# Optimization experiments

Hardware: AMD Instinct MI355X
Metric: run time of the kernel (lower is better)

## Reference

```python
import jax, jax.numpy as jnp
import numpy as np

MODEL_DIM = 1024
N_HEADS = 16
HEAD_DIM = 64  # q_dim == k_dim == v_dim


def setup_inputs() -> dict:
    key = jax.random.key(0)
    ks = jax.random.split(key, 7)
    B, S = 4, 2048
    scale = 1.0 / np.sqrt(MODEL_DIM)
    return {
        "q": jax.random.normal(ks[0], (B, S, MODEL_DIM), dtype=jnp.float32),
        "k": jax.random.normal(ks[1], (B, S, MODEL_DIM), dtype=jnp.float32),
        "v": jax.random.normal(ks[2], (B, S, MODEL_DIM), dtype=jnp.float32),
        # Linear weights stored as [out, in] like torch; no biases.
        "wq": jax.random.normal(ks[3], (N_HEADS * HEAD_DIM, MODEL_DIM), dtype=jnp.float32) * scale,
        "wk": jax.random.normal(ks[4], (N_HEADS * HEAD_DIM, MODEL_DIM), dtype=jnp.float32) * scale,
        "wv": jax.random.normal(ks[5], (N_HEADS * HEAD_DIM, MODEL_DIM), dtype=jnp.float32) * scale,
        "wo": jax.random.normal(ks[6], (MODEL_DIM, N_HEADS * HEAD_DIM), dtype=jnp.float32) * scale,
    }


def reference(q, k, v, wq, wk, wv, wo):
    B, Sq, _ = q.shape
    Sk = k.shape[1]
    # projections: [B,S,D] @ W^T -> [B,S,H*dh] -> [B,H,S,dh]
    qh = (q @ wq.T).reshape(B, Sq, N_HEADS, HEAD_DIM).transpose(0, 2, 1, 3)
    kh = (k @ wk.T).reshape(B, Sk, N_HEADS, HEAD_DIM).transpose(0, 2, 1, 3)
    vh = (v @ wv.T).reshape(B, Sk, N_HEADS, HEAD_DIM).transpose(0, 2, 1, 3)
    # scores [B,H,Sq,Sk], scaled by sqrt(k_dim)
    scores = jnp.einsum('bhqd,bhkd->bhqk', qh, kh) / jnp.sqrt(jnp.float32(HEAD_DIM))
    attn = jax.nn.softmax(scores, axis=-1)
    ctx = jnp.einsum('bhqk,bhkd->bhqd', attn, vh)  # [B,H,Sq,dh]
    ctx = ctx.transpose(0, 2, 1, 3).reshape(B, Sq, N_HEADS * HEAD_DIM)
    return ctx @ wo.T
```

## Files before the change

kernel.cpp:

```cpp
#include <hip/hip_runtime.h>
#include <cstdint>
#include <cstddef>


typedef _Float16 f16x8 __attribute__((ext_vector_type(8)));
typedef _Float16 f16x4 __attribute__((ext_vector_type(4)));
typedef _Float16 f16x2 __attribute__((ext_vector_type(2)));
typedef __fp16 h16x2 __attribute__((ext_vector_type(2)));
typedef float f32x4 __attribute__((ext_vector_type(4)));
typedef float f32x16 __attribute__((ext_vector_type(16)));
typedef unsigned u32x4 __attribute__((ext_vector_type(4)));
typedef int i32x2 __attribute__((ext_vector_type(2)));

#define LDS_CAST(p) ((__attribute__((address_space(3))) void*)(p))
#define GLB_CAST(p) ((const __attribute__((address_space(1))) void*)(p))

__device__ __forceinline__ void gload_lds16(const void* g, void* l) {
  __builtin_amdgcn_global_load_lds(GLB_CAST(g), LDS_CAST(l), 16, 0, 0);
}

__device__ __forceinline__ float fexp2(float x) {
#if __has_builtin(__builtin_amdgcn_exp2f)
  return __builtin_amdgcn_exp2f(x);
#else
  return exp2f(x);
#endif
}

__device__ __forceinline__ f16x2 pkrtz(float a, float b) {
  h16x2 r = __builtin_amdgcn_cvt_pkrtz(a, b);
  return __builtin_bit_cast(f16x2, r);
}

__device__ __forceinline__ float dot2acc(f16x2 a, float acc) {
#if __has_builtin(__builtin_amdgcn_fdot2)
  const f16x2 one2 = {(_Float16)1.0f, (_Float16)1.0f};
  return __builtin_amdgcn_fdot2(a, one2, acc, false);
#else
  return acc + (float)a[0] + (float)a[1];
#endif
}

__device__ __forceinline__ void pl32swap(unsigned& a, unsigned& b) {
#if __has_builtin(__builtin_amdgcn_permlane32_swap)
  i32x2 r = __builtin_amdgcn_permlane32_swap((int)a, (int)b, false, false);
  a = (unsigned)r[0];
  b = (unsigned)r[1];
#else
  asm("v_permlane32_swap_b32 %0, %1" : "+v"(a), "+v"(b));
#endif
}

__global__ void cvt_all(const float* __restrict__ q, const float* __restrict__ k,
                        const float* __restrict__ v, const float* __restrict__ wq,
                        const float* __restrict__ wk, const float* __restrict__ wv,
                        const float* __restrict__ wo, _Float16* __restrict__ oq,
                        _Float16* __restrict__ ok, _Float16* __restrict__ ov,
                        _Float16* __restrict__ owq, _Float16* __restrict__ owk,
                        _Float16* __restrict__ owv, _Float16* __restrict__ owo) {
  int id = blockIdx.x;
  const float* in;
  _Float16* out;
  int base;
  if (id < 24576) {
    int z = id >> 13;
    base = (id & 8191) * 256;
    in = z == 0 ? q : z == 1 ? k : v;
    out = z == 0 ? oq : z == 1 ? ok : ov;
  } else {
    int id2 = id - 24576;
    int z = id2 >> 10;
    base = (id2 & 1023) * 256;
    in = z == 0 ? wq : z == 1 ? wk : z == 2 ? wv : wo;
    out = z == 0 ? owq : z == 1 ? owk : z == 2 ? owv : owo;
  }
  int i = base + threadIdx.x;
  float4 vv = ((const float4*)in)[i];
  f16x4 o = {(_Float16)vv.x, (_Float16)vv.y, (_Float16)vv.z, (_Float16)vv.w};
  ((f16x4*)out)[i] = o;
}

template <int MODE>
__device__ __forceinline__ void gemm_core(const _Float16* __restrict__ A,
                                          const _Float16* __restrict__ W,
                                          void* __restrict__ C, float scale,
                                          _Float16* As, _Float16* Bs) {
  constexpr int K = 1024, N = 1024;
  const int tid = threadIdx.x;
  const int wid = tid >> 6;
  const int lane = tid & 63;
  const int quad = lane >> 4;
  const int l16 = lane & 15;
  const int wm = wid >> 1;
  const int wn = wid & 1;

  int lin = blockIdx.y * 8 + blockIdx.x;
  int swz = (lin & 7) * 64 + (lin >> 3);
  const int m0 = (swz >> 3) * 128;
  const int n0 = (swz & 7) * 128;

  const _Float16* Ag = A + (size_t)m0 * K;
  const _Float16* Bg = W + (size_t)n0 * K;

  f32x4 acc[4][4];
#pragma unroll
  for (int i = 0; i < 4; i++)
#pragma unroll
    for (int j = 0; j < 4; j++) acc[i][j] = (f32x4){0.f, 0.f, 0.f, 0.f};

  const int lrow = lane >> 2;
  const int swsrc = ((lane & 3) ^ ((lane >> 3) & 3)) * 8;

  auto stage = [&](_Float16* Ad, _Float16* Bd, int k0) {
#pragma unroll
    for (int i = 0; i < 2; i++) {
      int issue = wid * 2 + i;
      gload_lds16(Ag + (size_t)(issue * 16 + lrow) * K + k0 + swsrc,
                  Ad + issue * 512);
      gload_lds16(Bg + (size_t)(issue * 16 + lrow) * K + k0 + swsrc,
                  Bd + issue * 512);
    }
  };

  const int swq = (quad ^ ((l16 >> 1) & 3)) * 8;

  auto compute = [&](const _Float16* Ab, const _Float16* Bb) {
    f16x8 af[4], bfr[4];
#pragma unroll
    for (int mt = 0; mt < 4; mt++)
      af[mt] = *(const f16x8*)&Ab[(wm * 64 + mt * 16 + l16) * 32 + swq];
#pragma unroll
    for (int nt = 0; nt < 4; nt++)
      bfr[nt] = *(const f16x8*)&Bb[(wn * 64 + nt * 16 + l16) * 32 + swq];
#pragma unroll
    for (int mt = 0; mt < 4; mt++)
#pragma unroll
      for (int nt = 0; nt < 4; nt++)
        acc[mt][nt] = __builtin_amdgcn_mfma_f32_16x16x32_f16(
            af[mt], bfr[nt], acc[mt][nt], 0, 0, 0);
  };

  _Float16* A0 = As;
  _Float16* A1 = As + 4096;
  _Float16* B0 = Bs;
  _Float16* B1 = Bs + 4096;

  stage(A0, B0, 0);
  asm volatile("s_waitcnt vmcnt(0)" ::: "memory");
  __builtin_amdgcn_s_barrier();

  for (int g = 0; g < 15; g++) {
    int t2 = g * 2;
    stage(A1, B1, (t2 + 1) * 32);
    compute(A0, B0);
    asm volatile("s_waitcnt vmcnt(0)" ::: "memory");
    __builtin_amdgcn_s_barrier();
    stage(A0, B0, (t2 + 2) * 32);
    compute(A1, B1);
    asm volatile("s_waitcnt vmcnt(0)" ::: "memory");
    __builtin_amdgcn_s_barrier();
  }
  stage(A1, B1, 31 * 32);
  compute(A0, B0);
  asm volatile("s_waitcnt vmcnt(0)" ::: "memory");
  __builtin_amdgcn_s_barrier();
  compute(A1, B1);

#pragma unroll
  for (int mt = 0; mt < 4; mt++) {
#pragma unroll
    for (int nt = 0; nt < 4; nt++) {
#pragma unroll
      for (int r = 0; r < 4; r++) {
        int m = m0 + wm * 64 + mt * 16 + quad * 4 + r;
        int n = n0 + wn * 64 + nt * 16 + l16;
        float v = acc[mt][nt][r] * scale;
        if (MODE == 0) {
          ((float*)C)[(size_t)m * N + n] = v;
        } else {
          int b = m >> 11, s = m & 2047;
          int h = n >> 6, dd = n & 63;
          size_t bh = (size_t)(b * 16 + h);
          if (MODE == 1) {
            ((_Float16*)C)[(bh * 2048 + s) * 64 + dd] = (_Float16)v;
          } else if (MODE == 3) {
            int kt2 = s >> 5, l32k = s & 31;
            int s4 = dd >> 4, hi8 = (dd >> 3) & 1, j = dd & 7;
            size_t idx = (bh * 32 + (kt2 >> 1)) * 8192 +
                         (((kt2 & 1) * 4 + s4) * 512) + (hi8 * 32 + l32k) * 8 +
                         j;
            ((_Float16*)C)[idx] = (_Float16)v;
          } else {
            int kt = s >> 6, ks = (s >> 4) & 3, hi8 = (s >> 3) & 1, j = s & 7;
            int dt = dd >> 5, l32v = dd & 31;
            size_t idx = (bh * 32 + kt) * 8192 + 4096 + ((dt * 4 + ks) * 512) +
                         (hi8 * 32 + l32v) * 8 + j;
            ((_Float16*)C)[idx] = (_Float16)v;
          }
        }
      }
    }
  }
}

__global__ __launch_bounds__(256, 4) void gemm_qkv(
    const _Float16* __restrict__ qb, const _Float16* __restrict__ kb,
    const _Float16* __restrict__ vb, const _Float16* __restrict__ wq,
    const _Float16* __restrict__ wk, const _Float16* __restrict__ wv,
    _Float16* __restrict__ Qh, _Float16* __restrict__ KVf) {
  __shared__ _Float16 As[2 * 128 * 32];
  __shared__ _Float16 Bs[2 * 128 * 32];
  if (blockIdx.z == 0)
    gemm_core<1>(qb, wq, Qh, 0.18033688f, As, Bs);
  else if (blockIdx.z == 1)
    gemm_core<3>(kb, wk, KVf, 1.0f, As, Bs);
  else
    gemm_core<4>(vb, wv, KVf, 1.0f, As, Bs);
}

__global__ __launch_bounds__(256, 4) void gemm_wo(
    const _Float16* __restrict__ ctx, const _Float16* __restrict__ wo,
    float* __restrict__ out) {
  __shared__ _Float16 As[2 * 128 * 32];
  __shared__ _Float16 Bs[2 * 128 * 32];
  gemm_core<0>(ctx, wo, out, 1.0f, As, Bs);
}

__global__ __launch_bounds__(256, 3) void attn_kernel(
    const _Float16* __restrict__ Qh, const _Float16* __restrict__ KVf,
    _Float16* __restrict__ ctx) {
  __shared__ _Float16 sKV[3][8192];

  const int qt = blockIdx.x;
  const int bh = blockIdx.y;
  const int tid = threadIdx.x;
  const int wid = tid >> 6;
  const int lane = tid & 63;
  const int l32 = lane & 31;
  const int hi = lane >> 5;

  const _Float16* Qg = Qh + ((size_t)bh * 2048 + qt * 128 + wid * 32) * 64;
  const _Float16* KVb = KVf + (size_t)bh * 262144;

  f16x8 aq[4];
#pragma unroll
  for (int s = 0; s < 4; s++)
    aq[s] = *(const f16x8*)(Qg + (size_t)l32 * 64 + s * 16 + hi * 8);

  f32x16 acc[2];
#pragma unroll
  for (int i = 0; i < 16; i++) {
    acc[0][i] = 0.f;
    acc[1][i] = 0.f;
  }
  float lsA = 0.f, lsB = 0.f;

  auto stage = [&](int buf, int kt) {
    const _Float16* t = KVb + (size_t)kt * 8192;
#pragma unroll
    for (int i = 0; i < 4; i++) {
      int c = wid * 4 + i;
      gload_lds16(t + c * 512 + lane * 8, &sKV[buf][c * 512]);
    }
  };

  stage(0, 0);
  int cur = 0;

  for (int kt = 0; kt < 32; kt++) {
    int nxt = (cur == 2) ? 0 : cur + 1;
    if (kt < 31) {
      stage(nxt, kt + 1);
      asm volatile("s_waitcnt vmcnt(4)" ::: "memory");
    } else {
      asm volatile("s_waitcnt vmcnt(0)" ::: "memory");
    }
    __builtin_amdgcn_s_barrier();
    asm volatile("" ::: "memory");

    const _Float16* Ks = sKV[cur];
    const _Float16* Vs = sKV[cur] + 4096;

    f16x8 kf0[4], kf1[4];
#pragma unroll
    for (int s = 0; s < 4; s++) {
      kf0[s] = *(const f16x8*)&Ks[(0 * 4 + s) * 512 + lane * 8];
      kf1[s] = *(const f16x8*)&Ks[(4 + s) * 512 + lane * 8];
    }

    f32x16 s0, s1;
#pragma unroll
    for (int i = 0; i < 16; i++) {
      s0[i] = 0.f;
      s1[i] = 0.f;
    }
#pragma unroll
    for (int s = 0; s < 4; s++) {
      s0 = __builtin_amdgcn_mfma_f32_32x32x16_f16(kf0[s], aq[s], s0, 0, 0, 0);
      s1 = __builtin_amdgcn_mfma_f32_32x32x16_f16(kf1[s], aq[s], s1, 0, 0, 0);
    }

    f16x8 vf0[4], vf1[4];
#pragma unroll
    for (int g = 0; g < 4; g++) {
      vf0[g] = *(const f16x8*)&Vs[(0 * 4 + g) * 512 + lane * 8];
      vf1[g] = *(const f16x8*)&Vs[(4 + g) * 512 + lane * 8];
    }

    unsigned hw[2][8];
#pragma unroll
    for (int i = 0; i < 8; i++) {
      f16x2 hh = pkrtz(fexp2(s0[2 * i]), fexp2(s0[2 * i + 1]));
      if (i & 1)
        lsB = dot2acc(hh, lsB);
      else
        lsA = dot2acc(hh, lsA);
      hw[0][i] = __builtin_bit_cast(unsigned, hh);
    }
#pragma unroll
    for (int i = 0; i < 8; i++) {
      f16x2 hh = pkrtz(fexp2(s1[2 * i]), fexp2(s1[2 * i + 1]));
      if (i & 1)
        lsB = dot2acc(hh, lsB);
      else
        lsA = dot2acc(hh, lsA);
      hw[1][i] = __builtin_bit_cast(unsigned, hh);
    }

#pragma unroll
    for (int st = 0; st < 2; st++)
#pragma unroll
      for (int kh = 0; kh < 2; kh++) {
        unsigned w0 = hw[st][4 * kh + 0], w2 = hw[st][4 * kh + 2];
        unsigned w1 = hw[st][4 * kh + 1], w3 = hw[st][4 * kh + 3];
        pl32swap(w0, w2);
        pl32swap(w1, w3);
        u32x4 wv4 = {w0, w1, w2, w3};
        f16x8 pfrag = __builtin_bit_cast(f16x8, wv4);
        int g = st * 2 + kh;
        acc[0] = __builtin_amdgcn_mfma_f32_32x32x16_f16(vf0[g], pfrag, acc[0],
                                                        0, 0, 0);
        acc[1] = __builtin_amdgcn_mfma_f32_32x32x16_f16(vf1[g], pfrag, acc[1],
                                                        0, 0, 0);
      }

    cur = nxt;
  }

  float lsum = lsA + lsB;
  float l = lsum + __shfl_xor(lsum, 32);
  float inv = 1.f / l;
  const int b = bh >> 4, h = bh & 15;
  int q = qt * 128 + wid * 32 + l32;
  _Float16* outp = ctx + ((size_t)b * 2048 + q) * 1024 + h * 64;
#pragma unroll
  for (int dt = 0; dt < 2; dt++)
#pragma unroll
    for (int g = 0; g < 4; g++) {
      f16x4 o;
#pragma unroll
      for (int c = 0; c < 4; c++) o[c] = (_Float16)(acc[dt][g * 4 + c] * inv);
      *(f16x4*)(outp + dt * 32 + g * 8 + hi * 4) = o;
    }
}

extern "C" void kernel_launch(void* const* d_in, const int* in_sizes, int n_in,
                              void* d_out, int out_size, void* d_ws,
                              size_t ws_size, hipStream_t stream) {
  const float* q = (const float*)d_in[0];
  const float* k = (const float*)d_in[1];
  const float* v = (const float*)d_in[2];
  const float* wq = (const float*)d_in[3];
  const float* wk = (const float*)d_in[4];
  const float* wv = (const float*)d_in[5];
  const float* wo = (const float*)d_in[6];
  float* out = (float*)d_out;

  const size_t SD = (size_t)8192 * 1024;
  const size_t WSZ = (size_t)1024 * 1024;

  _Float16* ws = (_Float16*)d_ws;
  _Float16* qb = ws;
  _Float16* kb = ws + 1 * SD;
  _Float16* vb = ws + 2 * SD;
  _Float16* Qh = ws + 3 * SD;
  _Float16* KVf = ws + 4 * SD;
  _Float16* ctx = ws + 6 * SD;
  _Float16* wqb = ws + 7 * SD;
  _Float16* wkb = wqb + WSZ;
  _Float16* wvb = wqb + 2 * WSZ;
  _Float16* wob = wqb + 3 * WSZ;

  cvt_all<<<dim3(28672), 256, 0, stream>>>(q, k, v, wq, wk, wv, wo, qb, kb, vb,
                                           wqb, wkb, wvb, wob);

  gemm_qkv<<<dim3(8, 64, 3), 256, 0, stream>>>(qb, kb, vb, wqb, wkb, wvb, Qh,
                                               KVf);

  attn_kernel<<<dim3(16, 64), 256, 0, stream>>>(Qh, KVf, ctx);

  gemm_wo<<<dim3(8, 64), 256, 0, stream>>>(ctx, wob, out);
}
```

Measured before the change: 333.8 us.

## Switch attention to a two-buffer KV pipeline with higher occupancy and MFMA priority

The attention kernel's KV staging goes from a 3-deep rotating LDS ring to a 2-buffer ping-pong, and the loop is manually unrolled by two around a shared body lambda. Each tile now waits for all loads and hits a barrier. Halving LDS use lets launch bounds rise from 3 to 4 blocks per CU, so more waves can hide latency. s_setprio is raised around the MFMA blocks so waves in their matrix phase get issue priority. The trade-off is a shallower prefetch: the full vmcnt(0) wait each tile can expose load latency that the deeper ring used to hide.

```diff
diff --git a/kernel.cpp b/kernel.cpp
--- a/kernel.cpp
+++ b/kernel.cpp
@@ -226,10 +226,10 @@
   gemm_core<0>(ctx, wo, out, 1.0f, As, Bs);
 }
 
-__global__ __launch_bounds__(256, 3) void attn_kernel(
+__global__ __launch_bounds__(256, 4) void attn_kernel(
     const _Float16* __restrict__ Qh, const _Float16* __restrict__ KVf,
     _Float16* __restrict__ ctx) {
-  __shared__ _Float16 sKV[3][8192];
+  __shared__ _Float16 sKV[2][8192];
 
   const int qt = blockIdx.x;
   const int bh = blockIdx.y;
@@ -264,23 +264,8 @@
     }
   };
 
-  stage(0, 0);
-  int cur = 0;
-
-  for (int kt = 0; kt < 32; kt++) {
-    int nxt = (cur == 2) ? 0 : cur + 1;
-    if (kt < 31) {
-      stage(nxt, kt + 1);
-      asm volatile("s_waitcnt vmcnt(4)" ::: "memory");
-    } else {
-      asm volatile("s_waitcnt vmcnt(0)" ::: "memory");
-    }
-    __builtin_amdgcn_s_barrier();
-    asm volatile("" ::: "memory");
-
-    const _Float16* Ks = sKV[cur];
-    const _Float16* Vs = sKV[cur] + 4096;
-
+  auto body = [&](const _Float16* Ks) {
+    const _Float16* Vs = Ks + 4096;
     f16x8 kf0[4], kf1[4];
 #pragma unroll
     for (int s = 0; s < 4; s++) {
@@ -294,11 +279,13 @@
       s0[i] = 0.f;
       s1[i] = 0.f;
     }
+    __builtin_amdgcn_s_setprio(1);
 #pragma unroll
     for (int s = 0; s < 4; s++) {
       s0 = __builtin_amdgcn_mfma_f32_32x32x16_f16(kf0[s], aq[s], s0, 0, 0, 0);
       s1 = __builtin_amdgcn_mfma_f32_32x32x16_f16(kf1[s], aq[s], s1, 0, 0, 0);
     }
+    __builtin_amdgcn_s_setprio(0);
 
     f16x8 vf0[4], vf1[4];
 #pragma unroll
@@ -327,6 +314,7 @@
       hw[1][i] = __builtin_bit_cast(unsigned, hh);
     }
 
+    __builtin_amdgcn_s_setprio(1);
 #pragma unroll
     for (int st = 0; st < 2; st++)
 #pragma unroll
@@ -343,9 +331,33 @@
         acc[1] = __builtin_amdgcn_mfma_f32_32x32x16_f16(vf1[g], pfrag, acc[1],
                                                         0, 0, 0);
       }
-
-    cur = nxt;
+    __builtin_amdgcn_s_setprio(0);
+  };
+
+  stage(0, 0);
+  asm volatile("s_waitcnt vmcnt(0)" ::: "memory");
+  __builtin_amdgcn_s_barrier();
+  asm volatile("" ::: "memory");
+
+  for (int g = 0; g < 15; g++) {
+    int t2 = g * 2;
+    stage(1, t2 + 1);
+    body(sKV[0]);
+    asm volatile("s_waitcnt vmcnt(0)" ::: "memory");
+    __builtin_amdgcn_s_barrier();
+    asm volatile("" ::: "memory");
+    stage(0, t2 + 2);
+    body(sKV[1]);
+    asm volatile("s_waitcnt vmcnt(0)" ::: "memory");
+    __builtin_amdgcn_s_barrier();
+    asm volatile("" ::: "memory");
   }
+  stage(1, 31);
+  body(sKV[0]);
+  asm volatile("s_waitcnt vmcnt(0)" ::: "memory");
+  __builtin_amdgcn_s_barrier();
+  asm volatile("" ::: "memory");
+  body(sKV[1]);
 
   float lsum = lsA + lsB;
   float l = lsum + __shfl_xor(lsum, 32);
```

After: 353.5 us. 1.06x slower.

## Fuse fp32-to-fp16 activation conversion into QKV GEMM A-tile loading

Applied to the files above, without the earlier changes.

The separate pass that converted q, k, v activations to fp16 is removed. The QKV GEMM now loads fp32 A tiles into registers, converts them to fp16 and writes them into swizzled LDS, while the weights still arrive through direct global-to-LDS loads. This avoids writing and re-reading about 48MB of fp16 intermediates. In exchange, each GEMM block re-reads fp32 activations eight times across the N tiles (twice the bytes), and the A loads stall on vmcnt before the conversion, which weakens the overlap.

```diff
diff --git a/kernel.cpp b/kernel.cpp
--- a/kernel.cpp
+++ b/kernel.cpp
@@ -51,37 +51,22 @@
 #endif
 }
 
-__global__ void cvt_all(const float* __restrict__ q, const float* __restrict__ k,
-                        const float* __restrict__ v, const float* __restrict__ wq,
-                        const float* __restrict__ wk, const float* __restrict__ wv,
-                        const float* __restrict__ wo, _Float16* __restrict__ oq,
-                        _Float16* __restrict__ ok, _Float16* __restrict__ ov,
-                        _Float16* __restrict__ owq, _Float16* __restrict__ owk,
-                        _Float16* __restrict__ owv, _Float16* __restrict__ owo) {
+__global__ void cvt_w(const float* __restrict__ wq, const float* __restrict__ wk,
+                      const float* __restrict__ wv, const float* __restrict__ wo,
+                      _Float16* __restrict__ owq, _Float16* __restrict__ owk,
+                      _Float16* __restrict__ owv, _Float16* __restrict__ owo) {
   int id = blockIdx.x;
-  const float* in;
-  _Float16* out;
-  int base;
-  if (id < 24576) {
-    int z = id >> 13;
-    base = (id & 8191) * 256;
-    in = z == 0 ? q : z == 1 ? k : v;
-    out = z == 0 ? oq : z == 1 ? ok : ov;
-  } else {
-    int id2 = id - 24576;
-    int z = id2 >> 10;
-    base = (id2 & 1023) * 256;
-    in = z == 0 ? wq : z == 1 ? wk : z == 2 ? wv : wo;
-    out = z == 0 ? owq : z == 1 ? owk : z == 2 ? owv : owo;
-  }
-  int i = base + threadIdx.x;
-  float4 vv = ((const float4*)in)[i];
-  f16x4 o = {(_Float16)vv.x, (_Float16)vv.y, (_Float16)vv.z, (_Float16)vv.w};
+  int z = id >> 10;
+  const float* in = z == 0 ? wq : z == 1 ? wk : z == 2 ? wv : wo;
+  _Float16* out = z == 0 ? owq : z == 1 ? owk : z == 2 ? owv : owo;
+  int i = (id & 1023) * 256 + threadIdx.x;
+  float4 v = ((const float4*)in)[i];
+  f16x4 o = {(_Float16)v.x, (_Float16)v.y, (_Float16)v.z, (_Float16)v.w};
   ((f16x4*)out)[i] = o;
 }
 
-template <int MODE>
-__device__ __forceinline__ void gemm_core(const _Float16* __restrict__ A,
+template <int MODE, bool AF32>
+__device__ __forceinline__ void gemm_core(const void* __restrict__ Aptr,
                                           const _Float16* __restrict__ W,
                                           void* __restrict__ C, float scale,
                                           _Float16* As, _Float16* Bs) {
@@ -99,7 +84,8 @@
   const int m0 = (swz >> 3) * 128;
   const int n0 = (swz & 7) * 128;
 
-  const _Float16* Ag = A + (size_t)m0 * K;
+  const float* Ag32 = (const float*)Aptr + (size_t)m0 * K;
+  const _Float16* Ag16 = (const _Float16*)Aptr + (size_t)m0 * K;
   const _Float16* Bg = W + (size_t)n0 * K;
 
   f32x4 acc[4][4];
@@ -111,15 +97,42 @@
   const int lrow = lane >> 2;
   const int swsrc = ((lane & 3) ^ ((lane >> 3) & 3)) * 8;
 
-  auto stage = [&](_Float16* Ad, _Float16* Bd, int k0) {
+  auto stageAB16 = [&](_Float16* Ad, _Float16* Bd, int k0) {
 #pragma unroll
     for (int i = 0; i < 2; i++) {
       int issue = wid * 2 + i;
-      gload_lds16(Ag + (size_t)(issue * 16 + lrow) * K + k0 + swsrc,
+      gload_lds16(Ag16 + (size_t)(issue * 16 + lrow) * K + k0 + swsrc,
                   Ad + issue * 512);
       gload_lds16(Bg + (size_t)(issue * 16 + lrow) * K + k0 + swsrc,
                   Bd + issue * 512);
     }
+  };
+  auto stageB = [&](_Float16* Bd, int k0) {
+#pragma unroll
+    for (int i = 0; i < 2; i++) {
+      int issue = wid * 2 + i;
+      gload_lds16(Bg + (size_t)(issue * 16 + lrow) * K + k0 + swsrc,
+                  Bd + issue * 512);
+    }
+  };
+
+  const int r2 = tid >> 1;
+  const int hb = tid & 1;
+  auto loadA32 = [&](int k0, f32x4* ar) {
+#pragma unroll
+    for (int i = 0; i < 4; i++)
+      ar[i] = *(const f32x4*)&Ag32[(size_t)r2 * K + k0 + hb * 16 + i * 4];
+  };
+  auto cvtwriteA = [&](_Float16* Ad, const f32x4* ar) {
+    f16x8 o0 = {(_Float16)ar[0][0], (_Float16)ar[0][1], (_Float16)ar[0][2],
+                (_Float16)ar[0][3], (_Float16)ar[1][0], (_Float16)ar[1][1],
+                (_Float16)ar[1][2], (_Float16)ar[1][3]};
+    f16x8 o1 = {(_Float16)ar[2][0], (_Float16)ar[2][1], (_Float16)ar[2][2],
+                (_Float16)ar[2][3], (_Float16)ar[3][0], (_Float16)ar[3][1],
+                (_Float16)ar[3][2], (_Float16)ar[3][3]};
+    int x = (r2 >> 1) & 3;
+    *(f16x8*)&Ad[r2 * 32 + ((2 * hb) ^ x) * 8] = o0;
+    *(f16x8*)&Ad[r2 * 32 + ((2 * hb + 1) ^ x) * 8] = o1;
   };
 
   const int swq = (quad ^ ((l16 >> 1) & 3)) * 8;
@@ -145,26 +158,60 @@
   _Float16* B0 = Bs;
   _Float16* B1 = Bs + 4096;
 
-  stage(A0, B0, 0);
-  asm volatile("s_waitcnt vmcnt(0)" ::: "memory");
-  __builtin_amdgcn_s_barrier();
-
-  for (int g = 0; g < 15; g++) {
-    int t2 = g * 2;
-    stage(A1, B1, (t2 + 1) * 32);
+  if constexpr (AF32) {
+    f32x4 ar[4];
+    loadA32(0, ar);
+    stageB(B0, 0);
+    asm volatile("s_waitcnt vmcnt(0)" ::: "memory");
+    cvtwriteA(A0, ar);
+    asm volatile("s_waitcnt lgkmcnt(0)" ::: "memory");
+    __builtin_amdgcn_s_barrier();
+    for (int g = 0; g < 15; g++) {
+      int t2 = g * 2;
+      loadA32((t2 + 1) * 32, ar);
+      stageB(B1, (t2 + 1) * 32);
+      compute(A0, B0);
+      asm volatile("s_waitcnt vmcnt(0)" ::: "memory");
+      cvtwriteA(A1, ar);
+      asm volatile("s_waitcnt lgkmcnt(0)" ::: "memory");
+      __builtin_amdgcn_s_barrier();
+      loadA32((t2 + 2) * 32, ar);
+      stageB(B0, (t2 + 2) * 32);
+      compute(A1, B1);
+      asm volatile("s_waitcnt vmcnt(0)" ::: "memory");
+      cvtwriteA(A0, ar);
+      asm volatile("s_waitcnt lgkmcnt(0)" ::: "memory");
+      __builtin_amdgcn_s_barrier();
+    }
+    loadA32(31 * 32, ar);
+    stageB(B1, 31 * 32);
+    compute(A0, B0);
+    asm volatile("s_waitcnt vmcnt(0)" ::: "memory");
+    cvtwriteA(A1, ar);
+    asm volatile("s_waitcnt lgkmcnt(0)" ::: "memory");
+    __builtin_amdgcn_s_barrier();
+    compute(A1, B1);
+  } else {
+    stageAB16(A0, B0, 0);
+    asm volatile("s_waitcnt vmcnt(0)" ::: "memory");
+    __builtin_amdgcn_s_barrier();
+    for (int g = 0; g < 15; g++) {
+      int t2 = g * 2;
+      stageAB16(A1, B1, (t2 + 1) * 32);
+      compute(A0, B0);
+      asm volatile("s_waitcnt vmcnt(0)" ::: "memory");
+      __builtin_amdgcn_s_barrier();
+      stageAB16(A0, B0, (t2 + 2) * 32);
+      compute(A1, B1);
+      asm volatile("s_waitcnt vmcnt(0)" ::: "memory");
+      __builtin_amdgcn_s_barrier();
+    }
+    stageAB16(A1, B1, 31 * 32);
     compute(A0, B0);
     asm volatile("s_waitcnt vmcnt(0)" ::: "memory");
     __builtin_amdgcn_s_barrier();
-    stage(A0, B0, (t2 + 2) * 32);
     compute(A1, B1);
-    asm volatile("s_waitcnt vmcnt(0)" ::: "memory");
-    __builtin_amdgcn_s_barrier();
   }
-  stage(A1, B1, 31 * 32);
-  compute(A0, B0);
-  asm volatile("s_waitcnt vmcnt(0)" ::: "memory");
-  __builtin_amdgcn_s_barrier();
-  compute(A1, B1);
 
 #pragma unroll
   for (int mt = 0; mt < 4; mt++) {
@@ -204,18 +251,18 @@
 }
 
 __global__ __launch_bounds__(256, 4) void gemm_qkv(
-    const _Float16* __restrict__ qb, const _Float16* __restrict__ kb,
-    const _Float16* __restrict__ vb, const _Float16* __restrict__ wq,
+    const float* __restrict__ q, const float* __restrict__ k,
+    const float* __restrict__ v, const _Float16* __restrict__ wq,
     const _Float16* __restrict__ wk, const _Float16* __restrict__ wv,
     _Float16* __restrict__ Qh, _Float16* __restrict__ KVf) {
   __shared__ _Float16 As[2 * 128 * 32];
   __shared__ _Float16 Bs[2 * 128 * 32];
   if (blockIdx.z == 0)
-    gemm_core<1>(qb, wq, Qh, 0.18033688f, As, Bs);
+    gemm_core<1, true>(q, wq, Qh, 0.18033688f, As, Bs);
   else if (blockIdx.z == 1)
-    gemm_core<3>(kb, wk, KVf, 1.0f, As, Bs);
+    gemm_core<3, true>(k, wk, KVf, 1.0f, As, Bs);
   else
-    gemm_core<4>(vb, wv, KVf, 1.0f, As, Bs);
+    gemm_core<4, true>(v, wv, KVf, 1.0f, As, Bs);
 }
 
 __global__ __launch_bounds__(256, 4) void gemm_wo(
@@ -223,7 +270,7 @@
     float* __restrict__ out) {
   __shared__ _Float16 As[2 * 128 * 32];
   __shared__ _Float16 Bs[2 * 128 * 32];
-  gemm_core<0>(ctx, wo, out, 1.0f, As, Bs);
+  gemm_core<0, false>(ctx, wo, out, 1.0f, As, Bs);
 }
 
 __global__ __launch_bounds__(256, 3) void attn_kernel(
@@ -380,9 +427,6 @@
   const size_t WSZ = (size_t)1024 * 1024;
 
   _Float16* ws = (_Float16*)d_ws;
-  _Float16* qb = ws;
-  _Float16* kb = ws + 1 * SD;
-  _Float16* vb = ws + 2 * SD;
   _Float16* Qh = ws + 3 * SD;
   _Float16* KVf = ws + 4 * SD;
   _Float16* ctx = ws + 6 * SD;
@@ -391,10 +435,9 @@
   _Float16* wvb = wqb + 2 * WSZ;
   _Float16* wob = wqb + 3 * WSZ;
 
-  cvt_all<<<dim3(28672), 256, 0, stream>>>(q, k, v, wq, wk, wv, wo, qb, kb, vb,
-                                           wqb, wkb, wvb, wob);
-
-  gemm_qkv<<<dim3(8, 64, 3), 256, 0, stream>>>(qb, kb, vb, wqb, wkb, wvb, Qh,
+  cvt_w<<<dim3(4096), 256, 0, stream>>>(wq, wk, wv, wo, wqb, wkb, wvb, wob);
+
+  gemm_qkv<<<dim3(8, 64, 3), 256, 0, stream>>>(q, k, v, wqb, wkb, wvb, Qh,
                                                KVf);
 
   attn_kernel<<<dim3(16, 64), 256, 0, stream>>>(Qh, KVf, ctx);
```

Result: slower. 358.7 us (+7.5%).
